# Optimization experiments

Measured on AMD Instinct MI355X. Metric: run time of the kernel, lower is better.

## Reference

```python
import jax, jax.numpy as jnp
import numpy as np

B, S, H = 8, 1024, 768
NH, DH = 12, 64
F, E = 3072, 8
EPS = 1e-12

def layer_norm(x, g, b):
    mu = jnp.mean(x, axis=-1, keepdims=True)
    var = jnp.var(x, axis=-1, keepdims=True)
    return g * (x - mu) / jnp.sqrt(var + EPS) + b

def setup_inputs():
    key = jax.random.key(0)
    ks = jax.random.split(key, 20)
    std = 0.02
    d = {
        'hidden_states': jax.random.normal(ks[0], (B, S, H), jnp.float32),
        'Wq': jax.random.normal(ks[1], (H, H)) * std, 'bq': jnp.zeros((H,)),
        'Wk': jax.random.normal(ks[2], (H, H)) * std, 'bk': jnp.zeros((H,)),
        'Wv': jax.random.normal(ks[3], (H, H)) * std, 'bv': jnp.zeros((H,)),
        'Wao': jax.random.normal(ks[4], (H, H)) * std, 'bao': jnp.zeros((H,)),
        'ln1_g': jnp.ones((H,)), 'ln1_b': jnp.zeros((H,)),
        'Wr': jax.random.normal(ks[5], (H, E)) * std, 'br': jnp.zeros((E,)),
        'Wi': jax.random.normal(ks[6], (E, H, F)) * std, 'bi': jnp.zeros((E, F)),
        'Wo': jax.random.normal(ks[7], (F, H)) * std, 'bo': jnp.zeros((H,)),
        'ln2_g': jnp.ones((H,)), 'ln2_b': jnp.zeros((H,)),
    }
    return d

def reference(hidden_states, Wq, bq, Wk, bk, Wv, bv, Wao, bao, ln1_g, ln1_b,
              Wr, br, Wi, bi, Wo, bo, ln2_g, ln2_b):
    b, s, h = hidden_states.shape
    # --- self attention ---
    q = (hidden_states @ Wq + bq).reshape(b, s, NH, DH)
    k = (hidden_states @ Wk + bk).reshape(b, s, NH, DH)
    v = (hidden_states @ Wv + bv).reshape(b, s, NH, DH)
    scores = jnp.einsum('bqhd,bkhd->bhqk', q, k) / jnp.sqrt(jnp.float32(DH))
    probs = jax.nn.softmax(scores, axis=-1)
    ctx = jnp.einsum('bhqk,bkhd->bqhd', probs, v).reshape(b, s, h)
    attention_output = layer_norm(ctx @ Wao + bao + hidden_states, ln1_g, ln1_b)
    # --- router ---
    routing_scores = jax.nn.softmax(attention_output @ Wr + br, axis=-1)  # [b,s,E]
    routing_expert = jnp.argmax(routing_scores, axis=-1)  # [b,s]
    # --- expert FFN (dispatch/combine via per-expert masking) ---
    flat_x = attention_output.reshape(-1, h)          # [T,H]
    flat_e = routing_expert.reshape(-1)               # [T]
    flat_inter = jnp.zeros((b * s, F), flat_x.dtype)
    for e in range(E):
        mask = (flat_e == e)[:, None].astype(flat_x.dtype)
        y = jax.nn.gelu(flat_x @ Wi[e] + bi[e], approximate=False)
        flat_inter = flat_inter + mask * y
    inter = flat_inter.reshape(b, s, F)
    # --- output (dense + residual layernorm) ---
    layer_output = layer_norm(inter @ Wo + bo + attention_output, ln2_g, ln2_b)
    return layer_output, routing_scores
```

## Files before the change

kernel.cpp:

```cpp
#include <hip/hip_runtime.h>
#include <math.h>
#include <stdint.h>

#define TOKS 8192
#define HDIM 768
#define FDIM 3072
#define NEXP 8
#define NHEAD 12
#define SEQ 1024
#define BATCH 8
#define PERMSZ 9216

typedef __attribute__((ext_vector_type(8))) short s16x8;
typedef __attribute__((ext_vector_type(4))) short s16x4;
typedef __attribute__((ext_vector_type(4))) float f32x4;

__device__ __forceinline__ short f2bf(float f) {
  uint32_t u = __float_as_uint(f);
  uint32_t r = (u + 0x7fffu + ((u >> 16) & 1u)) >> 16;
  return (short)(r & 0xffffu);
}
__device__ __forceinline__ float bf2f(short h) {
  return __uint_as_float(((uint32_t)(uint16_t)h) << 16);
}
__device__ __forceinline__ void gload16(const void* g, void* l) {
  __builtin_amdgcn_global_load_lds(
      (const __attribute__((address_space(1))) uint32_t*)g,
      (__attribute__((address_space(3))) uint32_t*)l, 16, 0, 0);
}
__device__ __forceinline__ void pipe_wait_barrier() {
  asm volatile("s_waitcnt vmcnt(0)" ::: "memory");
  __builtin_amdgcn_s_barrier();
}

__global__ __launch_bounds__(256) void convert_split(
    const float* __restrict__ X, short* __restrict__ Xh, short* __restrict__ Xl, int n4)
{
  const int i = blockIdx.x * 256 + threadIdx.x;
  if (i >= n4) return;
  const float4 v = ((const float4*)X)[i];
  const float a[4] = {v.x, v.y, v.z, v.w};
  s16x4 h, l;
#pragma unroll
  for (int j = 0; j < 4; ++j) {
    h[j] = f2bf(a[j]);
    l[j] = f2bf(a[j] - bf2f(h[j]));
  }
  ((s16x4*)Xh)[i] = h;
  ((s16x4*)Xl)[i] = l;
}

__global__ __launch_bounds__(256) void transpose_split(
    const float* __restrict__ W, short* __restrict__ WTh, short* __restrict__ WTl,
    int K, int N)
{
  __shared__ float t[32][33];
  const int tid = threadIdx.x;
  const int tx = tid & 31, ty = tid >> 5;
  const int n0 = blockIdx.x * 32, k0 = blockIdx.y * 32;
#pragma unroll
  for (int r = 0; r < 4; ++r)
    t[ty + r * 8][tx] = W[(size_t)(k0 + ty + r * 8) * N + n0 + tx];
  __syncthreads();
#pragma unroll
  for (int r = 0; r < 4; ++r) {
    const float v = t[tx][ty + r * 8];
    const short h = f2bf(v);
    WTh[(size_t)(n0 + ty + r * 8) * K + k0 + tx] = h;
    WTl[(size_t)(n0 + ty + r * 8) * K + k0 + tx] = f2bf(v - bf2f(h));
  }
}

__global__ __launch_bounds__(256) void qkv_split_mfma(
    const short* __restrict__ Ah, const short* __restrict__ Al,
    const short* __restrict__ BhT, const short* __restrict__ BlT,
    const float* __restrict__ bias,
    short* __restrict__ QKh, short* __restrict__ QKl,
    short* __restrict__ VTh, short* __restrict__ VTl)
{
  const int K = 768;
  __shared__ __align__(16) short lAh[4096];
  __shared__ __align__(16) short lAl[4096];
  __shared__ __align__(16) short lBh[2][4096];
  __shared__ __align__(16) short lBl[2][4096];
  const int dsp = blockIdx.x + 18 * blockIdx.y;
  const int orig = (dsp & 7) * 144 + (dsp >> 3);
  const int bx = orig % 18, by = orig / 18;
  const int tid = threadIdx.x;
  const int w = tid >> 6, lane = tid & 63;
  const int wr = w >> 1, wc = w & 1;
  const int row0 = by * 128, col0 = bx * 128;
  const int sr = lane & 15, kg = lane >> 4;
  const size_t a0 = (size_t)(row0 + 2 * w * 16 + sr) * K + kg * 8;
  const size_t a1 = a0 + (size_t)16 * K;
  const size_t b0 = (size_t)(col0 + 2 * w * 16 + sr) * K + kg * 8;
  const size_t b1 = b0 + (size_t)16 * K;
  const int d0 = (2 * w) * 512, d1 = (2 * w + 1) * 512;
#define STAGE_QA(k0) do { \
    gload16(Ah + a0 + (k0), &lAh[d0]); \
    gload16(Ah + a1 + (k0), &lAh[d1]); \
    gload16(Al + a0 + (k0), &lAl[d0]); \
    gload16(Al + a1 + (k0), &lAl[d1]); \
  } while (0)
#define STAGE_QB(bu, k0) do { \
    gload16(BhT + b0 + (k0), &lBh[bu][d0]); \
    gload16(BhT + b1 + (k0), &lBh[bu][d1]); \
    gload16(BlT + b0 + (k0), &lBl[bu][d0]); \
    gload16(BlT + b1 + (k0), &lBl[bu][d1]); \
  } while (0)
  f32x4 acc[4][4] = {};
  STAGE_QA(0);
  STAGE_QB(0, 0);
  pipe_wait_barrier();
  int cur = 0;
  for (int t = 0; t < 24; ++t) {
    s16x8 ah[4], al[4], bh[4], bl[4];
#pragma unroll
    for (int i = 0; i < 4; ++i) {
      ah[i] = *(const s16x8*)&lAh[(wr * 4 + i) * 512 + lane * 8];
      al[i] = *(const s16x8*)&lAl[(wr * 4 + i) * 512 + lane * 8];
      bh[i] = *(const s16x8*)&lBh[cur][(wc * 4 + i) * 512 + lane * 8];
      bl[i] = *(const s16x8*)&lBl[cur][(wc * 4 + i) * 512 + lane * 8];
    }
    __syncthreads();
    if (t < 23) {
      STAGE_QA((t + 1) * 32);
      STAGE_QB(cur ^ 1, (t + 1) * 32);
    }
#pragma unroll
    for (int mi = 0; mi < 4; ++mi)
#pragma unroll
      for (int ni = 0; ni < 4; ++ni) {
        acc[mi][ni] = __builtin_amdgcn_mfma_f32_16x16x32_bf16(ah[mi], bh[ni], acc[mi][ni], 0, 0, 0);
        acc[mi][ni] = __builtin_amdgcn_mfma_f32_16x16x32_bf16(ah[mi], bl[ni], acc[mi][ni], 0, 0, 0);
        acc[mi][ni] = __builtin_amdgcn_mfma_f32_16x16x32_bf16(al[mi], bh[ni], acc[mi][ni], 0, 0, 0);
      }
    pipe_wait_barrier();
    cur ^= 1;
  }
#undef STAGE_QA
#undef STAGE_QB
  const int cl = lane & 15, rg = lane >> 4;
#pragma unroll
  for (int mi = 0; mi < 4; ++mi)
#pragma unroll
    for (int ni = 0; ni < 4; ++ni) {
      const int c = col0 + wc * 64 + ni * 16 + cl;
      const int rowb = row0 + wr * 64 + mi * 16 + rg * 4;
      const float qscale = (c < 768) ? 0.125f : 1.0f;
      s16x4 hv, lv;
#pragma unroll
      for (int r = 0; r < 4; ++r) {
        const float v = (acc[mi][ni][r] + bias[c]) * qscale;
        const short hh = f2bf(v);
        hv[r] = hh;
        lv[r] = f2bf(v - bf2f(hh));
      }
      if (c < 1536) {
#pragma unroll
        for (int r = 0; r < 4; ++r) {
          QKh[(size_t)(rowb + r) * 1536 + c] = hv[r];
          QKl[(size_t)(rowb + r) * 1536 + c] = lv[r];
        }
      } else {
        const int dall = c - 1536;
        const size_t vi = (((size_t)((rowb >> 10) * NHEAD + (dall >> 6))) * 64 + (dall & 63)) * 1024
                          + (rowb & 1023);
        *(s16x4*)(VTh + vi) = hv;
        *(s16x4*)(VTl + vi) = lv;
      }
    }
}

__global__ __launch_bounds__(256) void gemm_splitk_staged(
    const short* __restrict__ Ah, const short* __restrict__ Al,
    const short* __restrict__ BhT, const short* __restrict__ BlT,
    const float* __restrict__ bias, float* __restrict__ C0, float* __restrict__ C1,
    int N, int K)
{
  __shared__ __align__(16) short lAh[2][4096];
  __shared__ __align__(16) short lAl[2][4096];
  __shared__ __align__(16) short lBh[2][4096];
  __shared__ __align__(16) short lBl[2][4096];
  const int tid = threadIdx.x;
  const int w = tid >> 6, lane = tid & 63;
  const int wr = w >> 1, wc = w & 1;
  const int row0 = blockIdx.y * 128, col0 = blockIdx.x * 128;
  const int z = blockIdx.z;
  const int Khalf = K >> 1, koff = z * Khalf;
  const int sr = lane & 15, kg = lane >> 4;
  const size_t a0 = (size_t)(row0 + 2 * w * 16 + sr) * K + koff + kg * 8;
  const size_t a1 = a0 + (size_t)16 * K;
  const size_t b0 = (size_t)(col0 + 2 * w * 16 + sr) * K + koff + kg * 8;
  const size_t b1 = b0 + (size_t)16 * K;
  const int d0 = (2 * w) * 512, d1 = (2 * w + 1) * 512;
#define STAGE_K4(bu, k0) do { \
    gload16(Ah + a0 + (k0), &lAh[bu][d0]); \
    gload16(Ah + a1 + (k0), &lAh[bu][d1]); \
    gload16(Al + a0 + (k0), &lAl[bu][d0]); \
    gload16(Al + a1 + (k0), &lAl[bu][d1]); \
    gload16(BhT + b0 + (k0), &lBh[bu][d0]); \
    gload16(BhT + b1 + (k0), &lBh[bu][d1]); \
    gload16(BlT + b0 + (k0), &lBl[bu][d0]); \
    gload16(BlT + b1 + (k0), &lBl[bu][d1]); \
  } while (0)
  f32x4 acc[4][4] = {};
  const int NT = Khalf >> 5;
  STAGE_K4(0, 0);
  pipe_wait_barrier();
  int cur = 0;
  for (int t = 0; t < NT; ++t) {
    if (t + 1 < NT) STAGE_K4(cur ^ 1, (t + 1) * 32);
    s16x8 ah[4], al[4], bh[4], bl[4];
#pragma unroll
    for (int i = 0; i < 4; ++i) {
      ah[i] = *(const s16x8*)&lAh[cur][(wr * 4 + i) * 512 + lane * 8];
      al[i] = *(const s16x8*)&lAl[cur][(wr * 4 + i) * 512 + lane * 8];
      bh[i] = *(const s16x8*)&lBh[cur][(wc * 4 + i) * 512 + lane * 8];
      bl[i] = *(const s16x8*)&lBl[cur][(wc * 4 + i) * 512 + lane * 8];
    }
#pragma unroll
    for (int mi = 0; mi < 4; ++mi)
#pragma unroll
      for (int ni = 0; ni < 4; ++ni) {
        acc[mi][ni] = __builtin_amdgcn_mfma_f32_16x16x32_bf16(ah[mi], bh[ni], acc[mi][ni], 0, 0, 0);
        acc[mi][ni] = __builtin_amdgcn_mfma_f32_16x16x32_bf16(ah[mi], bl[ni], acc[mi][ni], 0, 0, 0);
        acc[mi][ni] = __builtin_amdgcn_mfma_f32_16x16x32_bf16(al[mi], bh[ni], acc[mi][ni], 0, 0, 0);
      }
    pipe_wait_barrier();
    cur ^= 1;
  }
#undef STAGE_K4
  float* C = z ? C1 : C0;
  const int cl = lane & 15, rg = lane >> 4;
#pragma unroll
  for (int mi = 0; mi < 4; ++mi)
#pragma unroll
    for (int r = 0; r < 4; ++r) {
      const int row = row0 + wr * 64 + mi * 16 + rg * 4 + r;
#pragma unroll
      for (int ni = 0; ni < 4; ++ni) {
        const int c = col0 + wc * 64 + ni * 16 + cl;
        C[(size_t)row * N + c] = acc[mi][ni][r] + (z ? 0.f : bias[c]);
      }
    }
}

__global__ __launch_bounds__(128, 2) void attention_part(
    const short* __restrict__ QKh, const short* __restrict__ QKl,
    const short* __restrict__ VTh, const short* __restrict__ VTl,
    float* __restrict__ O0, float* __restrict__ O1,
    float2* __restrict__ ml0, float2* __restrict__ ml1)
{
  __shared__ __align__(16) short lPh[2][2560];
  __shared__ __align__(16) short lPl[2][2560];
  const int tid = threadIdx.x;
  const int w = tid >> 6, lane = tid & 63;
  const int dsp = blockIdx.x + 32 * (blockIdx.y + 12 * blockIdx.z);
  const int orig = (dsp & 7) * 384 + (dsp >> 3);
  const int wx = orig & 31;
  const int b = orig / 384, h = (orig >> 5) % 12;
  const int z = wx & 1;
  const int q0 = (wx >> 1) * 64 + w * 32;
  const int kv0 = z * 512;
  const int sr = lane & 15, kg = lane >> 4;
  const int cl = sr, rg = kg;
  short* myPh = lPh[w];
  short* myPl = lPl[w];
  float* Op = z ? O1 : O0;
  float2* mlp = z ? ml1 : ml0;

  s16x8 qh[2][2], ql[2][2];
  {
    const size_t qbase = ((size_t)b * SEQ + q0 + sr) * 1536 + h * 64 + kg * 8;
#pragma unroll
    for (int mi = 0; mi < 2; ++mi)
#pragma unroll
      for (int ks = 0; ks < 2; ++ks) {
        const size_t o = qbase + (size_t)mi * (16 * 1536) + ks * 32;
        qh[mi][ks] = *(const s16x8*)(QKh + o);
        ql[mi][ks] = *(const s16x8*)(QKl + o);
      }
  }
  float m_run[2][4], l_run[2][4];
#pragma unroll
  for (int mi = 0; mi < 2; ++mi)
#pragma unroll
    for (int r = 0; r < 4; ++r) { m_run[mi][r] = -3.0e38f; l_run[mi][r] = 0.f; }
  f32x4 acc_o[2][4] = {};

  for (int kt = kv0; kt < kv0 + 512; kt += 64) {
    s16x8 kh[4][2], kl2[4][2];
    {
      const size_t kbase = ((size_t)b * SEQ + kt + sr) * 1536 + 768 + h * 64 + kg * 8;
#pragma unroll
      for (int ni = 0; ni < 4; ++ni)
#pragma unroll
        for (int ks = 0; ks < 2; ++ks) {
          const size_t o = kbase + (size_t)ni * (16 * 1536) + ks * 32;
          kh[ni][ks] = *(const s16x8*)(QKh + o);
          kl2[ni][ks] = *(const s16x8*)(QKl + o);
        }
    }
    f32x4 accs[2][4] = {};
    __builtin_amdgcn_s_setprio(1);
#pragma unroll
    for (int ks = 0; ks < 2; ++ks)
#pragma unroll
      for (int ni = 0; ni < 4; ++ni)
#pragma unroll
        for (int mi = 0; mi < 2; ++mi) {
          accs[mi][ni] = __builtin_amdgcn_mfma_f32_16x16x32_bf16(qh[mi][ks], kh[ni][ks], accs[mi][ni], 0, 0, 0);
          accs[mi][ni] = __builtin_amdgcn_mfma_f32_16x16x32_bf16(qh[mi][ks], kl2[ni][ks], accs[mi][ni], 0, 0, 0);
          accs[mi][ni] = __builtin_amdgcn_mfma_f32_16x16x32_bf16(ql[mi][ks], kh[ni][ks], accs[mi][ni], 0, 0, 0);
        }
    __builtin_amdgcn_s_setprio(0);
    s16x8 vh[4][2], vl2[4][2];
    {
      const size_t vbase = (((size_t)(b * NHEAD + h)) * 64 + sr) * 1024 + kt + kg * 8;
#pragma unroll
      for (int nd = 0; nd < 4; ++nd)
#pragma unroll
        for (int ks2 = 0; ks2 < 2; ++ks2) {
          const size_t o = vbase + (size_t)nd * (16 * 1024) + ks2 * 32;
          vh[nd][ks2] = *(const s16x8*)(VTh + o);
          vl2[nd][ks2] = *(const s16x8*)(VTl + o);
        }
    }
#pragma unroll
    for (int mi = 0; mi < 2; ++mi)
#pragma unroll
      for (int r = 0; r < 4; ++r) {
        float mx = fmaxf(fmaxf(accs[mi][0][r], accs[mi][1][r]),
                         fmaxf(accs[mi][2][r], accs[mi][3][r]));
        mx = fmaxf(mx, __shfl_xor(mx, 1));
        mx = fmaxf(mx, __shfl_xor(mx, 2));
        mx = fmaxf(mx, __shfl_xor(mx, 4));
        mx = fmaxf(mx, __shfl_xor(mx, 8));
        const float mn = fmaxf(m_run[mi][r], mx);
        const float c = __expf(m_run[mi][r] - mn);
        m_run[mi][r] = mn;
        l_run[mi][r] *= c;
#pragma unroll
        for (int nd = 0; nd < 4; ++nd) acc_o[mi][nd][r] *= c;
        float sum = 0.f;
#pragma unroll
        for (int ni = 0; ni < 4; ++ni) {
          const float p = __expf(accs[mi][ni][r] - mn);
          sum += p;
          const short hh = f2bf(p);
          const int idx = (mi * 2 + (ni >> 1)) * 640 + (rg * 4 + r) * 40 + (ni & 1) * 16 + cl;
          myPh[idx] = hh;
          myPl[idx] = f2bf(p - bf2f(hh));
        }
        sum += __shfl_xor(sum, 1);
        sum += __shfl_xor(sum, 2);
        sum += __shfl_xor(sum, 4);
        sum += __shfl_xor(sum, 8);
        l_run[mi][r] += sum;
      }
    __builtin_amdgcn_s_setprio(1);
#pragma unroll
    for (int ks2 = 0; ks2 < 2; ++ks2) {
      s16x8 pf[2], pg[2];
#pragma unroll
      for (int mi = 0; mi < 2; ++mi) {
        const int ra = (mi * 2 + ks2) * 640 + sr * 40 + kg * 8;
        pf[mi] = *(const s16x8*)&myPh[ra];
        pg[mi] = *(const s16x8*)&myPl[ra];
      }
#pragma unroll
      for (int nd = 0; nd < 4; ++nd)
#pragma unroll
        for (int mi = 0; mi < 2; ++mi) {
          acc_o[mi][nd] = __builtin_amdgcn_mfma_f32_16x16x32_bf16(pf[mi], vh[nd][ks2], acc_o[mi][nd], 0, 0, 0);
          acc_o[mi][nd] = __builtin_amdgcn_mfma_f32_16x16x32_bf16(pf[mi], vl2[nd][ks2], acc_o[mi][nd], 0, 0, 0);
          acc_o[mi][nd] = __builtin_amdgcn_mfma_f32_16x16x32_bf16(pg[mi], vh[nd][ks2], acc_o[mi][nd], 0, 0, 0);
        }
    }
    __builtin_amdgcn_s_setprio(0);
  }
#pragma unroll
  for (int mi = 0; mi < 2; ++mi)
#pragma unroll
    for (int nd = 0; nd < 4; ++nd)
#pragma unroll
      for (int r = 0; r < 4; ++r) {
        const int row = q0 + mi * 16 + rg * 4 + r;
        const int d = h * 64 + nd * 16 + cl;
        Op[((size_t)b * SEQ + row) * HDIM + d] = acc_o[mi][nd][r];
      }
  if (sr == 0) {
#pragma unroll
    for (int mi = 0; mi < 2; ++mi)
#pragma unroll
      for (int r = 0; r < 4; ++r) {
        const int row = q0 + mi * 16 + rg * 4 + r;
        mlp[(size_t)(b * NHEAD + h) * SEQ + row] = make_float2(m_run[mi][r], l_run[mi][r]);
      }
  }
}

__global__ __launch_bounds__(256) void combine_split(
    const float* __restrict__ O0, const float* __restrict__ O1,
    const float2* __restrict__ ml0, const float2* __restrict__ ml1,
    short* __restrict__ Ch, short* __restrict__ Cl)
{
  const int t = blockIdx.x;
  const int b = t >> 10, s = t & 1023;
  const int tid = threadIdx.x;
#pragma unroll
  for (int i = 0; i < 3; ++i) {
    const int idx = tid + i * 256;
    const int h = idx >> 6;
    const float2 a0 = ml0[(size_t)(b * NHEAD + h) * SEQ + s];
    const float2 a1 = ml1[(size_t)(b * NHEAD + h) * SEQ + s];
    const float mm = fmaxf(a0.x, a1.x);
    const float w0 = __expf(a0.x - mm), w1 = __expf(a1.x - mm);
    const float denom = a0.y * w0 + a1.y * w1;
    const size_t o = (size_t)t * HDIM + idx;
    const float v = (O0[o] * w0 + O1[o] * w1) / denom;
    const short hh = f2bf(v);
    Ch[o] = hh;
    Cl[o] = f2bf(v - bf2f(hh));
  }
}

__global__ __launch_bounds__(256) void convert_bf16(
    const float* __restrict__ X, short* __restrict__ Y, int n4)
{
  const int i = blockIdx.x * 256 + threadIdx.x;
  if (i >= n4) return;
  const float4 v = ((const float4*)X)[i];
  s16x4 s;
  s[0] = f2bf(v.x); s[1] = f2bf(v.y); s[2] = f2bf(v.z); s[3] = f2bf(v.w);
  ((s16x4*)Y)[i] = s;
}

__global__ __launch_bounds__(256) void transpose_to_bf16(
    const float* __restrict__ W, short* __restrict__ WT, int K, int N)
{
  const size_t off = (size_t)blockIdx.z * (size_t)K * N;
  const float* Wp = W + off;
  short* WTp = WT + off;
  __shared__ float t[32][33];
  const int tid = threadIdx.x;
  const int tx = tid & 31, ty = tid >> 5;
  const int n0 = blockIdx.x * 32, k0 = blockIdx.y * 32;
#pragma unroll
  for (int r = 0; r < 4; ++r)
    t[ty + r * 8][tx] = Wp[(size_t)(k0 + ty + r * 8) * N + n0 + tx];
  __syncthreads();
#pragma unroll
  for (int r = 0; r < 4; ++r)
    WTp[(size_t)(n0 + ty + r * 8) * K + k0 + tx] = f2bf(t[tx][ty + r * 8]);
}

__global__ __launch_bounds__(256) void expert_up_mfma(
    const short* __restrict__ Abf, const short* __restrict__ WiT,
    const float* __restrict__ bi, const int* __restrict__ perm,
    const int* __restrict__ offs, short* __restrict__ interb)
{
  const int row0 = blockIdx.x * 128;
  if (row0 >= offs[NEXP]) return;
  int e = 0;
  while (offs[e + 1] <= row0) ++e;
  __shared__ __align__(16) short lA[2][4096];
  __shared__ __align__(16) short lB[2][4096];
  __shared__ int toks[128];
  const int tid = threadIdx.x;
  const int w = tid >> 6, lane = tid & 63;
  const int wr = w >> 1, wc = w & 1;
  const int col0 = blockIdx.y * 128;
  if (tid < 128) toks[tid] = perm[row0 + tid];
  __syncthreads();
  const int sr = lane & 15, kg = lane >> 4;
  int t0 = toks[2 * w * 16 + sr];        if (t0 < 0) t0 = toks[0];
  int t1 = toks[(2 * w + 1) * 16 + sr];  if (t1 < 0) t1 = toks[0];
  const size_t a0 = (size_t)t0 * HDIM + kg * 8;
  const size_t a1 = (size_t)t1 * HDIM + kg * 8;
  const short* Bt = WiT + (size_t)e * FDIM * HDIM;
  const size_t b0 = (size_t)(col0 + 2 * w * 16 + sr) * HDIM + kg * 8;
  const size_t b1 = b0 + (size_t)16 * HDIM;
  const int d0 = (2 * w) * 512, d1 = (2 * w + 1) * 512;
#define STAGE_E(bu, k0) do { \
    gload16(Abf + a0 + (k0), &lA[bu][d0]); \
    gload16(Abf + a1 + (k0), &lA[bu][d1]); \
    gload16(Bt + b0 + (k0), &lB[bu][d0]); \
    gload16(Bt + b1 + (k0), &lB[bu][d1]); \
  } while (0)
  f32x4 acc[4][4] = {};
  STAGE_E(0, 0);
  pipe_wait_barrier();
  int cur = 0;
  for (int t = 0; t < 24; ++t) {
    if (t < 23) STAGE_E(cur ^ 1, (t + 1) * 32);
    s16x8 af[4], bg[4];
#pragma unroll
    for (int i = 0; i < 4; ++i) {
      af[i] = *(const s16x8*)&lA[cur][(wr * 4 + i) * 512 + lane * 8];
      bg[i] = *(const s16x8*)&lB[cur][(wc * 4 + i) * 512 + lane * 8];
    }
#pragma unroll
    for (int mi = 0; mi < 4; ++mi)
#pragma unroll
      for (int ni = 0; ni < 4; ++ni)
        acc[mi][ni] = __builtin_amdgcn_mfma_f32_16x16x32_bf16(af[mi], bg[ni], acc[mi][ni], 0, 0, 0);
    pipe_wait_barrier();
    cur ^= 1;
  }
#undef STAGE_E
  const int cl = lane & 15, rg = lane >> 4;
#pragma unroll
  for (int mi = 0; mi < 4; ++mi) {
#pragma unroll
    for (int r = 0; r < 4; ++r) {
      const int rl = wr * 64 + mi * 16 + rg * 4 + r;
      const int tok = toks[rl];
      if (tok < 0) continue;
#pragma unroll
      for (int ni = 0; ni < 4; ++ni) {
        const int c = col0 + wc * 64 + ni * 16 + cl;
        float v = acc[mi][ni][r] + bi[(size_t)e * FDIM + c];
        v = 0.5f * v * (1.0f + erff(v * 0.70710678118654752f));
        interb[(size_t)tok * FDIM + c] = f2bf(v);
      }
    }
  }
}

__global__ __launch_bounds__(256) void wo_mfma(
    const short* __restrict__ Ab, const short* __restrict__ BT,
    const float* __restrict__ bias, float* __restrict__ C0, float* __restrict__ C1)
{
  __shared__ __align__(16) short lA[2][4096];
  __shared__ __align__(16) short lB[2][4096];
  const int tid = threadIdx.x;
  const int w = tid >> 6, lane = tid & 63;
  const int wr = w >> 1, wc = w & 1;
  const int row0 = blockIdx.y * 128, col0 = blockIdx.x * 128;
  const int z = blockIdx.z;
  const int kbase = z * 1536;
  const int sr = lane & 15, kg = lane >> 4;
  const size_t a0 = (size_t)(row0 + 2 * w * 16 + sr) * FDIM + kbase + kg * 8;
  const size_t a1 = a0 + (size_t)16 * FDIM;
  const size_t b0 = (size_t)(col0 + 2 * w * 16 + sr) * FDIM + kbase + kg * 8;
  const size_t b1 = b0 + (size_t)16 * FDIM;
  const int d0 = (2 * w) * 512, d1 = (2 * w + 1) * 512;
#define STAGE_W(bu, k0) do { \
    gload16(Ab + a0 + (k0), &lA[bu][d0]); \
    gload16(Ab + a1 + (k0), &lA[bu][d1]); \
    gload16(BT + b0 + (k0), &lB[bu][d0]); \
    gload16(BT + b1 + (k0), &lB[bu][d1]); \
  } while (0)
  f32x4 acc[4][4] = {};
  STAGE_W(0, 0);
  pipe_wait_barrier();
  int cur = 0;
  for (int t = 0; t < 48; ++t) {
    if (t < 47) STAGE_W(cur ^ 1, (t + 1) * 32);
    s16x8 af[4], bg[4];
#pragma unroll
    for (int i = 0; i < 4; ++i) {
      af[i] = *(const s16x8*)&lA[cur][(wr * 4 + i) * 512 + lane * 8];
      bg[i] = *(const s16x8*)&lB[cur][(wc * 4 + i) * 512 + lane * 8];
    }
#pragma unroll
    for (int mi = 0; mi < 4; ++mi)
#pragma unroll
      for (int ni = 0; ni < 4; ++ni)
        acc[mi][ni] = __builtin_amdgcn_mfma_f32_16x16x32_bf16(af[mi], bg[ni], acc[mi][ni], 0, 0, 0);
    pipe_wait_barrier();
    cur ^= 1;
  }
#undef STAGE_W
  float* C = z ? C1 : C0;
  const int cl = lane & 15, rg = lane >> 4;
#pragma unroll
  for (int mi = 0; mi < 4; ++mi) {
#pragma unroll
    for (int r = 0; r < 4; ++r) {
      const int row = row0 + wr * 64 + mi * 16 + rg * 4 + r;
#pragma unroll
      for (int ni = 0; ni < 4; ++ni) {
        const int c = col0 + wc * 64 + ni * 16 + cl;
        C[(size_t)row * HDIM + c] = acc[mi][ni][r] + (z ? 0.f : bias[c]);
      }
    }
  }
}

__global__ __launch_bounds__(256) void add2_ln_kernel(
    const float* __restrict__ X1, const float* __restrict__ X2,
    const float* __restrict__ R, const float* __restrict__ g,
    const float* __restrict__ bb, float* __restrict__ out)
{
  const int t = blockIdx.x;
  const int tid = threadIdx.x;
  const float* x1 = X1 + (size_t)t * HDIM;
  const float* x2 = X2 + (size_t)t * HDIM;
  const float* r = R + (size_t)t * HDIM;
  float v[3];
  float sum = 0.f, ssq = 0.f;
#pragma unroll
  for (int i = 0; i < 3; ++i) {
    const float val = x1[tid + i * 256] + x2[tid + i * 256] + r[tid + i * 256];
    v[i] = val;
    sum += val;
    ssq += val * val;
  }
#pragma unroll
  for (int o = 32; o > 0; o >>= 1) {
    sum += __shfl_down(sum, o);
    ssq += __shfl_down(ssq, o);
  }
  __shared__ float red[10];
  const int wid = tid >> 6, lane = tid & 63;
  if (lane == 0) { red[wid] = sum; red[4 + wid] = ssq; }
  __syncthreads();
  if (tid == 0) {
    const float s = red[0] + red[1] + red[2] + red[3];
    const float q = red[4] + red[5] + red[6] + red[7];
    const float mean = s * (1.f / HDIM);
    const float var = q * (1.f / HDIM) - mean * mean;
    red[8] = mean;
    red[9] = rsqrtf(fmaxf(var, 0.f) + 1e-12f);
  }
  __syncthreads();
  const float mean = red[8], rstd = red[9];
#pragma unroll
  for (int i = 0; i < 3; ++i) {
    const int idx = tid + i * 256;
    out[(size_t)t * HDIM + idx] = g[idx] * (v[i] - mean) * rstd + bb[idx];
  }
}

__global__ __launch_bounds__(256) void router_kernel(
    const float* __restrict__ X, const float* __restrict__ Wr,
    const float* __restrict__ br, float* __restrict__ scores_out,
    int* __restrict__ expert, int* __restrict__ counts)
{
  const int wid = threadIdx.x >> 6, lane = threadIdx.x & 63;
  const int tok = blockIdx.x * 4 + wid;
  const float* x = X + (size_t)tok * HDIM;
  float acc[8] = {};
  for (int k0 = 0; k0 < HDIM; k0 += 64) {
    const float xv = x[k0 + lane];
    const float* wrow = Wr + (size_t)(k0 + lane) * NEXP;
    const float4 w0 = *reinterpret_cast<const float4*>(wrow);
    const float4 w1 = *reinterpret_cast<const float4*>(wrow + 4);
    acc[0] = fmaf(xv, w0.x, acc[0]);
    acc[1] = fmaf(xv, w0.y, acc[1]);
    acc[2] = fmaf(xv, w0.z, acc[2]);
    acc[3] = fmaf(xv, w0.w, acc[3]);
    acc[4] = fmaf(xv, w1.x, acc[4]);
    acc[5] = fmaf(xv, w1.y, acc[5]);
    acc[6] = fmaf(xv, w1.z, acc[6]);
    acc[7] = fmaf(xv, w1.w, acc[7]);
  }
#pragma unroll
  for (int e = 0; e < 8; ++e)
#pragma unroll
    for (int o = 32; o > 0; o >>= 1) acc[e] += __shfl_down(acc[e], o);
  if (lane == 0) {
    float mx = -3.0e38f;
#pragma unroll
    for (int e = 0; e < 8; ++e) { acc[e] += br[e]; mx = fmaxf(mx, acc[e]); }
    float sum = 0.f;
#pragma unroll
    for (int e = 0; e < 8; ++e) { acc[e] = expf(acc[e] - mx); sum += acc[e]; }
    const float inv = 1.f / sum;
    int best = 0;
    float bv = acc[0];
#pragma unroll
    for (int e = 0; e < 8; ++e) {
      const float p = acc[e] * inv;
      scores_out[(size_t)tok * NEXP + e] = p;
      if (acc[e] > bv) { bv = acc[e]; best = e; }
    }
    expert[tok] = best;
    atomicAdd(&counts[best], 1);
  }
}

__global__ void offsets_kernel(const int* __restrict__ counts, int* __restrict__ offs)
{
  if (threadIdx.x == 0 && blockIdx.x == 0) {
    int a = 0;
    for (int e = 0; e < NEXP; ++e) {
      offs[e] = a;
      a += ((counts[e] + 127) >> 7) << 7;
    }
    offs[NEXP] = a;
  }
}

__global__ __launch_bounds__(256) void scatter_kernel(
    const int* __restrict__ expert, const int* __restrict__ offs,
    int* __restrict__ cursor, int* __restrict__ perm)
{
  const int t = blockIdx.x * 256 + threadIdx.x;
  if (t >= TOKS) return;
  const int e = expert[t];
  const int pos = atomicAdd(&cursor[e], 1);
  perm[offs[e] + pos] = t;
}

extern "C" void kernel_launch(void* const* d_in, const int* in_sizes, int n_in,
                              void* d_out, int out_size, void* d_ws, size_t ws_size,
                              hipStream_t stream) {
  const float* hidden = (const float*)d_in[0];
  const float* Wq  = (const float*)d_in[1];
  const float* bq  = (const float*)d_in[2];
  const float* Wk  = (const float*)d_in[3];
  const float* bk  = (const float*)d_in[4];
  const float* Wv  = (const float*)d_in[5];
  const float* bv  = (const float*)d_in[6];
  const float* Wao = (const float*)d_in[7];
  const float* bao = (const float*)d_in[8];
  const float* ln1g = (const float*)d_in[9];
  const float* ln1b = (const float*)d_in[10];
  const float* Wr  = (const float*)d_in[11];
  const float* br  = (const float*)d_in[12];
  const float* Wi  = (const float*)d_in[13];
  const float* bi  = (const float*)d_in[14];
  const float* Wo  = (const float*)d_in[15];
  const float* bo  = (const float*)d_in[16];
  const float* ln2g = (const float*)d_in[17];
  const float* ln2b = (const float*)d_in[18];

  float* out = (float*)d_out;
  float* scores_out = out + (size_t)TOKS * HDIM;

  const size_t M1 = (size_t)TOKS * HDIM;
  const size_t HW = (size_t)HDIM * HDIM;
  float* ws = (float*)d_ws;
  short* QKhb = (short*)ws;
  short* QKlb = (short*)(ws + M1);
  short* VThb = (short*)(ws + 2 * M1);
  short* VTlb = VThb + (size_t)BATCH * NHEAD * 64 * 1024;
  float* O0b  = ws + 3 * M1;
  float* O1b  = ws + 4 * M1;
  float* bqkv = ws + 3 * M1;
  short* Hh = (short*)(ws + 4 * M1);
  short* Hl = Hh + M1;
  short* Ch = (short*)(ws + 2 * M1);
  short* Cl = Ch + M1;
  short* wt = (short*)(ws + 5 * M1);
  short* WqkvhT = wt;
  short* WqkvlT = wt + 3 * HW;
  short* WaohT  = wt + 6 * HW;
  short* WaolT  = wt + 7 * HW;
  float2* ml0 = (float2*)(ws + 5 * M1 + 4 * HW);
  float2* ml1 = ml0 + (size_t)BATCH * NHEAD * SEQ;
  float* aoproj0  = ws;
  float* aoproj1  = ws + 3 * M1;
  float* attn_out = ws + M1;
  float* tmp2a    = ws;
  float* tmp2b    = ws + 3 * M1;
  short* Abf    = (short*)(ws + 2 * M1);
  short* WiT    = Abf + M1;
  short* WoT    = WiT + (size_t)NEXP * FDIM * HDIM;
  short* interb = WoT + (size_t)HDIM * FDIM;
  int* ints   = (int*)(interb + (size_t)TOKS * FDIM);
  int* perm   = ints;
  int* expert = ints + PERMSZ;
  int* counts = expert + TOKS;
  int* offs   = counts + NEXP;
  int* cursor = offs + NEXP + 1;

  hipMemsetAsync(counts, 0, (NEXP + NEXP + 1 + NEXP) * sizeof(int), stream);
  hipMemsetAsync(perm, 0xFF, PERMSZ * sizeof(int), stream);
  hipMemcpyAsync(bqkv,        bq, HDIM * sizeof(float), hipMemcpyDeviceToDevice, stream);
  hipMemcpyAsync(bqkv + 768,  bk, HDIM * sizeof(float), hipMemcpyDeviceToDevice, stream);
  hipMemcpyAsync(bqkv + 1536, bv, HDIM * sizeof(float), hipMemcpyDeviceToDevice, stream);

  const dim3 blk(256);
  convert_split<<<dim3(TOKS * HDIM / 4 / 256), blk, 0, stream>>>(hidden, Hh, Hl, TOKS * HDIM / 4);
  transpose_split<<<dim3(24, 24), blk, 0, stream>>>(Wq,  WqkvhT,          WqkvlT,          HDIM, HDIM);
  transpose_split<<<dim3(24, 24), blk, 0, stream>>>(Wk,  WqkvhT + HW,     WqkvlT + HW,     HDIM, HDIM);
  transpose_split<<<dim3(24, 24), blk, 0, stream>>>(Wv,  WqkvhT + 2 * HW, WqkvlT + 2 * HW, HDIM, HDIM);
  transpose_split<<<dim3(24, 24), blk, 0, stream>>>(Wao, WaohT,           WaolT,           HDIM, HDIM);

  qkv_split_mfma<<<dim3(2304 / 128, TOKS / 128), blk, 0, stream>>>(
      Hh, Hl, WqkvhT, WqkvlT, bqkv, QKhb, QKlb, VThb, VTlb);

  attention_part<<<dim3((SEQ / 64) * 2, NHEAD, BATCH), dim3(128), 0, stream>>>(
      QKhb, QKlb, VThb, VTlb, O0b, O1b, ml0, ml1);
  combine_split<<<dim3(TOKS), blk, 0, stream>>>(O0b, O1b, ml0, ml1, Ch, Cl);

  gemm_splitk_staged<<<dim3(HDIM / 128, TOKS / 128, 2), blk, 0, stream>>>(
      Ch, Cl, WaohT, WaolT, bao, aoproj0, aoproj1, HDIM, HDIM);
  add2_ln_kernel<<<dim3(TOKS), blk, 0, stream>>>(aoproj0, aoproj1, hidden, ln1g, ln1b, attn_out);

  router_kernel<<<dim3(TOKS / 4), blk, 0, stream>>>(attn_out, Wr, br, scores_out, expert, counts);
  offsets_kernel<<<dim3(1), dim3(64), 0, stream>>>(counts, offs);
  scatter_kernel<<<dim3(TOKS / 256), blk, 0, stream>>>(expert, offs, cursor, perm);

  transpose_to_bf16<<<dim3(FDIM / 32, HDIM / 32, NEXP), blk, 0, stream>>>(Wi, WiT, HDIM, FDIM);
  transpose_to_bf16<<<dim3(HDIM / 32, FDIM / 32, 1), blk, 0, stream>>>(Wo, WoT, FDIM, HDIM);
  convert_bf16<<<dim3(TOKS * HDIM / 4 / 256), blk, 0, stream>>>(attn_out, Abf, TOKS * HDIM / 4);

  expert_up_mfma<<<dim3(PERMSZ / 128, FDIM / 128), blk, 0, stream>>>(
      Abf, WiT, bi, perm, offs, interb);
  wo_mfma<<<dim3(HDIM / 128, TOKS / 128, 2), blk, 0, stream>>>(interb, WoT, bo, tmp2a, tmp2b);
  add2_ln_kernel<<<dim3(TOKS), blk, 0, stream>>>(tmp2a, tmp2b, attn_out, ln2g, ln2b, out);
}
```

Baseline: 861.7 us.

## Drop low-half split of softmax probabilities and fuse bf16 conversion into LayerNorm

In the attention kernel, probabilities are now stored only as a single bf16 value instead of a hi/lo pair. This removes one LDS buffer, its stores and loads, and one of the three MFMAs per PV step. The row sum is accumulated from the rounded values so normalization stays consistent, at the cost of lower precision in the P·V product. Separately, the first LayerNorm kernel now also writes a bf16 copy of its output, so the standalone convert_bf16 launch and its extra read of the activations are removed.

Measured after the change: 865.0 us. Within noise of the previous version (+0.4%).

```diff
diff --git a/kernel.cpp b/kernel.cpp
--- a/kernel.cpp
+++ b/kernel.cpp
@@ -253,7 +253,6 @@
     float2* __restrict__ ml0, float2* __restrict__ ml1)
 {
   __shared__ __align__(16) short lPh[2][2560];
-  __shared__ __align__(16) short lPl[2][2560];
   const int tid = threadIdx.x;
   const int w = tid >> 6, lane = tid & 63;
   const int dsp = blockIdx.x + 32 * (blockIdx.y + 12 * blockIdx.z);
@@ -266,7 +265,6 @@
   const int sr = lane & 15, kg = lane >> 4;
   const int cl = sr, rg = kg;
   short* myPh = lPh[w];
-  short* myPl = lPl[w];
   float* Op = z ? O1 : O0;
   float2* mlp = z ? ml1 : ml0;
 
@@ -347,11 +345,10 @@
 #pragma unroll
         for (int ni = 0; ni < 4; ++ni) {
           const float p = __expf(accs[mi][ni][r] - mn);
-          sum += p;
           const short hh = f2bf(p);
+          sum += bf2f(hh);
           const int idx = (mi * 2 + (ni >> 1)) * 640 + (rg * 4 + r) * 40 + (ni & 1) * 16 + cl;
           myPh[idx] = hh;
-          myPl[idx] = f2bf(p - bf2f(hh));
         }
         sum += __shfl_xor(sum, 1);
         sum += __shfl_xor(sum, 2);
@@ -362,12 +359,11 @@
     __builtin_amdgcn_s_setprio(1);
 #pragma unroll
     for (int ks2 = 0; ks2 < 2; ++ks2) {
-      s16x8 pf[2], pg[2];
+      s16x8 pf[2];
 #pragma unroll
       for (int mi = 0; mi < 2; ++mi) {
         const int ra = (mi * 2 + ks2) * 640 + sr * 40 + kg * 8;
         pf[mi] = *(const s16x8*)&myPh[ra];
-        pg[mi] = *(const s16x8*)&myPl[ra];
       }
 #pragma unroll
       for (int nd = 0; nd < 4; ++nd)
@@ -375,7 +371,6 @@
         for (int mi = 0; mi < 2; ++mi) {
           acc_o[mi][nd] = __builtin_amdgcn_mfma_f32_16x16x32_bf16(pf[mi], vh[nd][ks2], acc_o[mi][nd], 0, 0, 0);
           acc_o[mi][nd] = __builtin_amdgcn_mfma_f32_16x16x32_bf16(pf[mi], vl2[nd][ks2], acc_o[mi][nd], 0, 0, 0);
-          acc_o[mi][nd] = __builtin_amdgcn_mfma_f32_16x16x32_bf16(pg[mi], vh[nd][ks2], acc_o[mi][nd], 0, 0, 0);
         }
     }
     __builtin_amdgcn_s_setprio(0);
@@ -424,17 +419,6 @@
     Ch[o] = hh;
     Cl[o] = f2bf(v - bf2f(hh));
   }
-}
-
-__global__ __launch_bounds__(256) void convert_bf16(
-    const float* __restrict__ X, short* __restrict__ Y, int n4)
-{
-  const int i = blockIdx.x * 256 + threadIdx.x;
-  if (i >= n4) return;
-  const float4 v = ((const float4*)X)[i];
-  s16x4 s;
-  s[0] = f2bf(v.x); s[1] = f2bf(v.y); s[2] = f2bf(v.z); s[3] = f2bf(v.w);
-  ((s16x4*)Y)[i] = s;
 }
 
 __global__ __launch_bounds__(256) void transpose_to_bf16(
@@ -632,6 +616,53 @@
   for (int i = 0; i < 3; ++i) {
     const int idx = tid + i * 256;
     out[(size_t)t * HDIM + idx] = g[idx] * (v[i] - mean) * rstd + bb[idx];
+  }
+}
+
+__global__ __launch_bounds__(256) void add2_ln_bf16_kernel(
+    const float* __restrict__ X1, const float* __restrict__ X2,
+    const float* __restrict__ R, const float* __restrict__ g,
+    const float* __restrict__ bb, float* __restrict__ out, short* __restrict__ outb)
+{
+  const int t = blockIdx.x;
+  const int tid = threadIdx.x;
+  const float* x1 = X1 + (size_t)t * HDIM;
+  const float* x2 = X2 + (size_t)t * HDIM;
+  const float* r = R + (size_t)t * HDIM;
+  float v[3];
+  float sum = 0.f, ssq = 0.f;
+#pragma unroll
+  for (int i = 0; i < 3; ++i) {
+    const float val = x1[tid + i * 256] + x2[tid + i * 256] + r[tid + i * 256];
+    v[i] = val;
+    sum += val;
+    ssq += val * val;
+  }
+#pragma unroll
+  for (int o = 32; o > 0; o >>= 1) {
+    sum += __shfl_down(sum, o);
+    ssq += __shfl_down(ssq, o);
+  }
+  __shared__ float red[10];
+  const int wid = tid >> 6, lane = tid & 63;
+  if (lane == 0) { red[wid] = sum; red[4 + wid] = ssq; }
+  __syncthreads();
+  if (tid == 0) {
+    const float s = red[0] + red[1] + red[2] + red[3];
+    const float q = red[4] + red[5] + red[6] + red[7];
+    const float mean = s * (1.f / HDIM);
+    const float var = q * (1.f / HDIM) - mean * mean;
+    red[8] = mean;
+    red[9] = rsqrtf(fmaxf(var, 0.f) + 1e-12f);
+  }
+  __syncthreads();
+  const float mean = red[8], rstd = red[9];
+#pragma unroll
+  for (int i = 0; i < 3; ++i) {
+    const int idx = tid + i * 256;
+    const float o = g[idx] * (v[i] - mean) * rstd + bb[idx];
+    out[(size_t)t * HDIM + idx] = o;
+    outb[(size_t)t * HDIM + idx] = f2bf(o);
   }
 }
 
@@ -791,7 +822,8 @@
 
   gemm_splitk_staged<<<dim3(HDIM / 128, TOKS / 128, 2), blk, 0, stream>>>(
       Ch, Cl, WaohT, WaolT, bao, aoproj0, aoproj1, HDIM, HDIM);
-  add2_ln_kernel<<<dim3(TOKS), blk, 0, stream>>>(aoproj0, aoproj1, hidden, ln1g, ln1b, attn_out);
+  add2_ln_bf16_kernel<<<dim3(TOKS), blk, 0, stream>>>(
+      aoproj0, aoproj1, hidden, ln1g, ln1b, attn_out, Abf);
 
   router_kernel<<<dim3(TOKS / 4), blk, 0, stream>>>(attn_out, Wr, br, scores_out, expert, counts);
   offsets_kernel<<<dim3(1), dim3(64), 0, stream>>>(counts, offs);
@@ -799,7 +831,6 @@
 
   transpose_to_bf16<<<dim3(FDIM / 32, HDIM / 32, NEXP), blk, 0, stream>>>(Wi, WiT, HDIM, FDIM);
   transpose_to_bf16<<<dim3(HDIM / 32, FDIM / 32, 1), blk, 0, stream>>>(Wo, WoT, FDIM, HDIM);
-  convert_bf16<<<dim3(TOKS * HDIM / 4 / 256), blk, 0, stream>>>(attn_out, Abf, TOKS * HDIM / 4);
 
   expert_up_mfma<<<dim3(PERMSZ / 128, FDIM / 128), blk, 0, stream>>>(
       Abf, WiT, bi, perm, offs, interb);
```
